# Kernel tuning notes

Hardware: AMD Instinct MI355X
Metric: run time of the kernel (lower is better)

The kernel has to match this reference:

```python
import jax, jax.numpy as jnp
import numpy as np

SCALES = (1, 2, 4)
KS = 5          # conv kernel size
POOL = 2        # maxpool kernel & stride


def coarse_grain(x, s):
    # non-overlapping mean pool along last axis
    B, C, L = x.shape
    Lc = L // s
    return x[:, :, : Lc * s].reshape(B, C, Lc, s).mean(axis=-1)


def conv1d(x, w, b):
    # x: [B, C_in, L], w: [C_out, C_in, K] (torch layout), VALID padding, stride 1
    y = jax.lax.conv_general_dilated(
        x, w, window_strides=(1,), padding='VALID',
        dimension_numbers=('NCH', 'OIH', 'NCH'))
    return y + b[None, :, None]


def maxpool1d(x, k):
    B, C, L = x.shape
    Lp = L // k
    return x[:, :, : Lp * k].reshape(B, C, Lp, k).max(axis=-1)


def conv_block(x, w1, b1, w2, b2):
    x = maxpool1d(jax.nn.relu(conv1d(x, w1, b1)), POOL)
    x = maxpool1d(jax.nn.relu(conv1d(x, w2, b2)), POOL)
    return x


def setup_inputs() -> dict:
    key = jax.random.key(0)
    ks = jax.random.split(key, 9)
    B, C, NWL = 2048, 4, 480
    C1, C2 = 16, 32
    # flatten size per model's own arithmetic: sum over scales of conv/pool output lens * C2
    F = (117 + 57 + 27) * C2  # 6432
    NOUT = 5
    sc = lambda fan_in: 1.0 / np.sqrt(fan_in)
    return {
        'x':  jax.random.normal(ks[0], (B, C, NWL), dtype=jnp.float32),
        'w1': jax.random.uniform(ks[1], (C1, C, KS), jnp.float32, -sc(C * KS), sc(C * KS)),
        'b1': jax.random.uniform(ks[2], (C1,), jnp.float32, -sc(C * KS), sc(C * KS)),
        'w2': jax.random.uniform(ks[3], (C2, C1, KS), jnp.float32, -sc(C1 * KS), sc(C1 * KS)),
        'b2': jax.random.uniform(ks[4], (C2,), jnp.float32, -sc(C1 * KS), sc(C1 * KS)),
        'wl': jax.random.uniform(ks[5], (F, F), jnp.float32, -sc(F), sc(F)),
        'bl': jax.random.uniform(ks[6], (F,), jnp.float32, -sc(F), sc(F)),
        'wo': jax.random.uniform(ks[7], (NOUT, F), jnp.float32, -sc(F), sc(F)),
        'bo': jax.random.uniform(ks[8], (NOUT,), jnp.float32, -sc(F), sc(F)),
    }


def reference(x, w1, b1, w2, b2, wl, bl, wo, bo):
    # multi-scale feature mapping: shared ConvBlock applied to each coarse-grained scale
    feats = [conv_block(coarse_grain(x, s), w1, b1, w2, b2) for s in SCALES]
    f = jnp.concatenate(feats, axis=-1)            # [B, 32, 201]
    f = f.reshape(f.shape[0], -1)                  # [B, 6432]
    # the SAME linear layer (shared weights) is applied 4 times in torch
    for _ in range(4):
        f = jax.nn.relu(f @ wl.T + bl)
    return f @ wo.T + bo                           # [B, 5]
```

## Files before the change

### kernel.cpp

```cpp
#include <hip/hip_runtime.h>

typedef _Float16 v8h __attribute__((ext_vector_type(8)));
typedef _Float16 v4h __attribute__((ext_vector_type(4)));
typedef float    v4f __attribute__((ext_vector_type(4)));

#define GK 6432
#define GN 6432
#define GM 2048
#define KP 6528

__global__ void convert_w(const float* __restrict__ wl, _Float16* __restrict__ Wh)
{
    const int row = blockIdx.y;
    const int col = (blockIdx.x * 256 + threadIdx.x) * 4;
    if (col >= KP) return;
    v4h h;
    if (col < GK) {
        const float4 f = *(const float4*)(wl + (long)row * GK + col);
        h[0] = (_Float16)f.x; h[1] = (_Float16)f.y;
        h[2] = (_Float16)f.z; h[3] = (_Float16)f.w;
    } else {
        h[0] = (_Float16)0.f; h[1] = (_Float16)0.f;
        h[2] = (_Float16)0.f; h[3] = (_Float16)0.f;
    }
    *(v4h*)(Wh + (long)row * KP + col) = h;
}

#define SX   0
#define SX2  2048
#define SX4  3136
#define SW1  3712
#define SB1  4032
#define SW2  4048
#define SB2  6608
#define SP1  6640
#define LDSZ 13808

__global__ __launch_bounds__(256) void conv_feat(
    const float* __restrict__ x,
    const float* __restrict__ w1, const float* __restrict__ b1,
    const float* __restrict__ w2, const float* __restrict__ b2,
    _Float16* __restrict__ F0)
{
    __shared__ float lds[LDSZ];
    const int tid = threadIdx.x;
    const long b  = blockIdx.x;

    for (int i = tid; i < 1920; i += 256) {
        int c = i / 480, t = i % 480;
        lds[SX + c * 512 + t] = x[(b * 4 + c) * 480 + t];
    }
    for (int i = tid; i < 320;  i += 256) lds[SW1 + i] = w1[i];
    for (int i = tid; i < 16;   i += 256) lds[SB1 + i] = b1[i];
    for (int i = tid; i < 2560; i += 256) lds[SW2 + i] = w2[i];
    for (int i = tid; i < 32;   i += 256) lds[SB2 + i] = b2[i];
    for (int i = tid; i < KP - GK; i += 256) F0[b * KP + GK + i] = (_Float16)0.f;
    __syncthreads();

    for (int i = tid; i < 960; i += 256) {
        int c = i / 240, t = i % 240;
        lds[SX2 + c * 272 + t] = 0.5f * (lds[SX + c * 512 + 2 * t] + lds[SX + c * 512 + 2 * t + 1]);
    }
    for (int i = tid; i < 480; i += 256) {
        int c = i / 120, t = i % 120;
        float s = lds[SX + c * 512 + 4 * t]     + lds[SX + c * 512 + 4 * t + 1]
                + lds[SX + c * 512 + 4 * t + 2] + lds[SX + c * 512 + 4 * t + 3];
        lds[SX4 + c * 144 + t] = 0.25f * s;
    }
    __syncthreads();

    for (int jid = tid; jid < 16 * 34; jid += 256) {
        const int c1 = jid / 34, rid = jid % 34;
        const int sidx = (rid < 19) ? 0 : (rid < 29 ? 1 : 2);
        const int r0   = (sidx == 0) ? rid : (sidx == 1 ? rid - 19 : rid - 29);
        const int u0   = r0 * 13;
        const int xbase  = (sidx == 0) ? SX  : (sidx == 1 ? SX2 : SX4);
        const int xpitch = (sidx == 0) ? 512 : (sidx == 1 ? 272 : 144);
        const int P      = (sidx == 0) ? 238 : (sidx == 1 ? 118 : 58);
        const int pofs   = (sidx == 0) ? 0   : (sidx == 1 ? 238 : 356);

        float acc[26];
        const float bias = lds[SB1 + c1];
        #pragma unroll
        for (int i = 0; i < 26; ++i) acc[i] = bias;

        #pragma unroll
        for (int ci = 0; ci < 4; ++ci) {
            float w[30];
            const float* xr = &lds[xbase + ci * xpitch + 2 * u0];
            #pragma unroll
            for (int q = 0; q < 15; ++q) {
                float2 t2 = *(const float2*)(xr + 2 * q);
                w[2 * q] = t2.x; w[2 * q + 1] = t2.y;
            }
            float wt[5];
            #pragma unroll
            for (int k = 0; k < 5; ++k) wt[k] = lds[SW1 + (c1 * 4 + ci) * 5 + k];
            #pragma unroll
            for (int i = 0; i < 26; ++i) {
                #pragma unroll
                for (int k = 0; k < 5; ++k) acc[i] += w[i + k] * wt[k];
            }
        }
        #pragma unroll
        for (int i = 0; i < 13; ++i) {
            int u = u0 + i;
            if (u < P)
                lds[SP1 + c1 * 448 + pofs + u] = fmaxf(fmaxf(acc[2 * i], acc[2 * i + 1]), 0.f);
        }
    }
    __syncthreads();

    for (int jid = tid; jid < 32 * 17; jid += 256) {
        const int c2 = jid / 17, rid = jid % 17;
        const int sidx = (rid < 9) ? 0 : (rid < 14 ? 1 : 2);
        const int r0   = (sidx == 0) ? rid : (sidx == 1 ? rid - 9 : rid - 14);
        const int v0   = r0 * 13;
        const int pbase = (sidx == 0) ? 0   : (sidx == 1 ? 238 : 356);
        const int Pv    = (sidx == 0) ? 117 : (sidx == 1 ? 57  : 27);
        const int vout  = (sidx == 0) ? 0   : (sidx == 1 ? 117 : 174);

        float acc[26];
        const float bias = lds[SB2 + c2];
        #pragma unroll
        for (int i = 0; i < 26; ++i) acc[i] = bias;

        for (int c1 = 0; c1 < 16; ++c1) {
            float w[30];
            const float* pr = &lds[SP1 + c1 * 448 + pbase + 2 * v0];
            #pragma unroll
            for (int q = 0; q < 15; ++q) {
                float2 t2 = *(const float2*)(pr + 2 * q);
                w[2 * q] = t2.x; w[2 * q + 1] = t2.y;
            }
            float wt[5];
            #pragma unroll
            for (int k = 0; k < 5; ++k) wt[k] = lds[SW2 + (c2 * 16 + c1) * 5 + k];
            #pragma unroll
            for (int i = 0; i < 26; ++i) {
                #pragma unroll
                for (int k = 0; k < 5; ++k) acc[i] += w[i + k] * wt[k];
            }
        }
        #pragma unroll
        for (int i = 0; i < 13; ++i) {
            int v = v0 + i;
            if (v < Pv) {
                float f = fmaxf(fmaxf(acc[2 * i], acc[2 * i + 1]), 0.f);
                F0[b * KP + c2 * 201 + vout + v] = (_Float16)f;
            }
        }
    }
}

__global__ __launch_bounds__(512, 2) void gemm8(
    const _Float16* __restrict__ A, const _Float16* __restrict__ Bw,
    const float* __restrict__ bias, _Float16* __restrict__ C)
{
    __shared__ _Float16 sA[2][256 * 64];
    __shared__ _Float16 sB[2][256 * 64];

    const int tid  = threadIdx.x;
    const int lane = tid & 63;
    const int wave = tid >> 6;
    const int wr   = wave >> 2;
    const int wc   = wave & 3;

    const int id  = blockIdx.x;
    const long tile_m = (long)(id & 7) << 8;
    const long tile_n = (long)(id >> 3) << 8;

    const int lrow = lane >> 3;
    const int lcol = ((lane & 7) ^ lrow) << 3;

    const int arow = wr * 128 + wc * 32;
    const int brow = wc * 64 + wr * 32;
    const _Float16* pA = A + (tile_m + arow + lrow) * (long)KP + lcol;
    long br0 = tile_n + brow + lrow;
    long br1 = br0 + 8, br2 = br0 + 16, br3 = br0 + 24;
    if (br0 > 6431) br0 = 6431;
    if (br1 > 6431) br1 = 6431;
    if (br2 > 6431) br2 = 6431;
    if (br3 > 6431) br3 = 6431;
    const _Float16* pB0 = Bw + br0 * (long)KP + lcol;
    const _Float16* pB1 = Bw + br1 * (long)KP + lcol;
    const _Float16* pB2 = Bw + br2 * (long)KP + lcol;
    const _Float16* pB3 = Bw + br3 * (long)KP + lcol;

    const int aDst = arow * 64;
    const int bDst = brow * 64;

#define GLD(p, d) __builtin_amdgcn_global_load_lds(                          \
        (const __attribute__((address_space(1))) void*)(p),                  \
        (__attribute__((address_space(3))) void*)(d), 16, 0, 0)

#define STAGE_A4(SBUF, KO) {                                                 \
    GLD(pA + (KO),            &sA[SBUF][aDst]);                              \
    GLD(pA + (KO) +  8L * KP, &sA[SBUF][aDst +  512]);                       \
    GLD(pA + (KO) + 16L * KP, &sA[SBUF][aDst + 1024]);                       \
    GLD(pA + (KO) + 24L * KP, &sA[SBUF][aDst + 1536]); }

#define STAGE_B4(SBUF, KO) {                                                 \
    GLD(pB0 + (KO), &sB[SBUF][bDst]);                                        \
    GLD(pB1 + (KO), &sB[SBUF][bDst +  512]);                                 \
    GLD(pB2 + (KO), &sB[SBUF][bDst + 1024]);                                 \
    GLD(pB3 + (KO), &sB[SBUF][bDst + 1536]); }

    const int fr = lane & 15;
    const int fp = lane >> 4;
    const int sw = fr & 7;
    const int slot0 = ((fp)     ^ sw) << 3;
    const int slot1 = ((fp + 4) ^ sw) << 3;
    const int abase = (wr * 128 + fr) * 64;
    const int boffS = (wc * 64 + fr) * 64 + wr * 2048;
    const int boffO = (wc * 64 + fr) * 64 + (1 - wr) * 2048;

    v8h af[4][2], bfO[2][2], bfs0[2][2], bfs1[2][2];
    v4f accS[8][2], accO[8][2];
    #pragma unroll
    for (int m = 0; m < 8; ++m) {
        #pragma unroll
        for (int ni = 0; ni < 2; ++ni) {
            v4f z = {0.f, 0.f, 0.f, 0.f};
            accS[m][ni] = z; accO[m][ni] = z;
        }
    }

#define LDA(CA, H) { _Pragma("unroll")                                       \
    for (int mi = 0; mi < 4; ++mi) {                                         \
        af[mi][0] = *(const v8h*)&(CA)[abase + (H) * 4096 + mi * 1024 + slot0]; \
        af[mi][1] = *(const v8h*)&(CA)[abase + (H) * 4096 + mi * 1024 + slot1]; \
    } }

#define LDBF(CB, BOFF, D) {                                                  \
    D[0][0] = *(const v8h*)&(CB)[(BOFF) + slot0];                            \
    D[0][1] = *(const v8h*)&(CB)[(BOFF) + slot1];                            \
    D[1][0] = *(const v8h*)&(CB)[(BOFF) + 1024 + slot0];                     \
    D[1][1] = *(const v8h*)&(CB)[(BOFF) + 1024 + slot1]; }

#define MMAQ(ACC, MH, BF) { _Pragma("unroll")                                \
    for (int mi = 0; mi < 4; ++mi) { _Pragma("unroll")                       \
        for (int ni = 0; ni < 2; ++ni) {                                     \
            ACC[(MH)*4+mi][ni] = __builtin_amdgcn_mfma_f32_16x16x32_f16(     \
                af[mi][0], BF[ni][0], ACC[(MH)*4+mi][ni], 0, 0, 0);          \
            ACC[(MH)*4+mi][ni] = __builtin_amdgcn_mfma_f32_16x16x32_f16(     \
                af[mi][1], BF[ni][1], ACC[(MH)*4+mi][ni], 0, 0, 0);          \
        } } }

#define ROUND(CA, CB, CBN, SBUF, KO, BFS, BFSN, S2, RA) {                    \
                                           \
    LDA(CA, 0);                                                              \
    __builtin_amdgcn_s_barrier();                                            \
    asm volatile("s_waitcnt lgkmcnt(0)" ::: "memory");                       \
    __builtin_amdgcn_s_setprio(1);                                           \
    MMAQ(accS, 0, BFS);                                                      \
    __builtin_amdgcn_s_setprio(0);                                           \
    __builtin_amdgcn_s_barrier();                                            \
                    \
    LDBF(CB, boffO, bfO);                                                    \
    if ((S2) && wc < 2) STAGE_A4(SBUF, KO);                                  \
    __builtin_amdgcn_s_barrier();                                            \
    asm volatile("s_waitcnt lgkmcnt(0)" ::: "memory");                       \
    __builtin_amdgcn_s_setprio(1);                                           \
    MMAQ(accO, 0, bfO);                                                      \
    __builtin_amdgcn_s_setprio(0);                                           \
    __builtin_amdgcn_s_barrier();                                            \
                            \
    LDA(CA, 1);                                                              \
    if (S2) STAGE_B4(SBUF, KO);                                              \
    __builtin_amdgcn_s_barrier();                                            \
    asm volatile("s_waitcnt lgkmcnt(0)" ::: "memory");                       \
    __builtin_amdgcn_s_setprio(1);                                           \
    MMAQ(accO, 1, bfO);                                                      \
    __builtin_amdgcn_s_setprio(0);                                           \
    __builtin_amdgcn_s_barrier();                                            \
    \
    if ((S2) && wc >= 2) STAGE_A4(SBUF, KO);                                 \
    __builtin_amdgcn_s_barrier();                                            \
    __builtin_amdgcn_s_setprio(1);                                           \
    MMAQ(accS, 1, BFS);                                                      \
    __builtin_amdgcn_s_setprio(0);                                           \
    if (S2) { asm volatile("s_waitcnt vmcnt(8)" ::: "memory"); }             \
    else    { asm volatile("s_waitcnt vmcnt(0)" ::: "memory"); }             \
    if (RA) LDBF(CBN, boffS, BFSN);                                          \
    __builtin_amdgcn_sched_barrier(0);                                       \
    __builtin_amdgcn_s_barrier(); }

    STAGE_A4(0, 0);  STAGE_B4(0, 0);
    STAGE_A4(1, 64); STAGE_B4(1, 64);
    pA += 128; pB0 += 128; pB1 += 128; pB2 += 128; pB3 += 128;
    asm volatile("s_waitcnt vmcnt(8)" ::: "memory");
    __builtin_amdgcn_s_barrier();
    LDBF(sB[0], boffS, bfs0);

    for (int kt = 0; kt < 102; kt += 2) {
        const bool s2a = kt < 100;
        const bool s2b = kt < 99;
        const bool raB = kt < 100;
        ROUND(sA[0], sB[0], sB[1], 0, 0,  bfs0, bfs1, s2a, true);
        ROUND(sA[1], sB[1], sB[0], 1, 64, bfs1, bfs0, s2b, raB);
        pA += 128; pB0 += 128; pB1 += 128; pB2 += 128; pB3 += 128;
    }

#define EPI(ACC, COL0) { _Pragma("unroll")                                   \
    for (int ni = 0; ni < 2; ++ni) {                                         \
        const long col = (COL0) + ni * 16;                                   \
        if (col < KP) {                                                      \
            const bool val = col < GN;                                       \
            const float bv = val ? bias[col] : 0.f;                          \
            _Pragma("unroll")                                                \
            for (int m = 0; m < 8; ++m) {                                    \
                const long row = tile_m + wr * 128 + m * 16 + fp * 4;        \
                _Pragma("unroll")                                            \
                for (int r = 0; r < 4; ++r) {                                \
                    float v = ACC[m][ni][r] + bv;                            \
                    v = v > 0.f ? v : 0.f;                                   \
                    C[(row + r) * (long)KP + col] = val ? (_Float16)v        \
                                                        : (_Float16)0.f;     \
                }                                                            \
            }                                                                \
        }                                                                    \
    } }

    const long colS0 = tile_n + wc * 64 + wr * 32 + fr;
    const long colO0 = tile_n + wc * 64 + (1 - wr) * 32 + fr;
    EPI(accS, colS0);
    EPI(accO, colO0);

#undef GLD
#undef STAGE_A4
#undef STAGE_B4
#undef LDA
#undef LDBF
#undef MMAQ
#undef ROUND
#undef EPI
}

__global__ __launch_bounds__(256) void final_out(
    const _Float16* __restrict__ F, const float* __restrict__ wo,
    const float* __restrict__ bo, float* __restrict__ out)
{
    __shared__ float red[4][8];
    const long b   = blockIdx.x;
    const int tid  = threadIdx.x;
    const int lane = tid & 63;
    const int wave = tid >> 6;
    float acc[5] = {0.f, 0.f, 0.f, 0.f, 0.f};
    const _Float16* f = F + b * KP;

    const int c1 = (wave + 1) * 402;
    for (int c = wave * 402 + lane; c < c1; c += 64) {
        const int k = c << 2;
        v4h f4 = *(const v4h*)(f + k);
        const float f0 = (float)f4[0], f1 = (float)f4[1];
        const float f2 = (float)f4[2], f3 = (float)f4[3];
        #pragma unroll
        for (int o = 0; o < 5; ++o) {
            const float4 w4 = *(const float4*)(wo + o * GK + k);
            acc[o] += f0 * w4.x + f1 * w4.y + f2 * w4.z + f3 * w4.w;
        }
    }
    #pragma unroll
    for (int o = 0; o < 5; ++o) {
        #pragma unroll
        for (int off = 32; off > 0; off >>= 1) acc[o] += __shfl_down(acc[o], off, 64);
    }
    if (lane == 0) {
        #pragma unroll
        for (int o = 0; o < 5; ++o) red[wave][o] = acc[o];
    }
    __syncthreads();
    if (tid < 5)
        out[b * 5 + tid] = red[0][tid] + red[1][tid] + red[2][tid] + red[3][tid] + bo[tid];
}

extern "C" void kernel_launch(void* const* d_in, const int* in_sizes, int n_in,
                              void* d_out, int out_size, void* d_ws, size_t ws_size,
                              hipStream_t stream)
{
    const float* x  = (const float*)d_in[0];
    const float* w1 = (const float*)d_in[1];
    const float* b1 = (const float*)d_in[2];
    const float* w2 = (const float*)d_in[3];
    const float* b2 = (const float*)d_in[4];
    const float* wl = (const float*)d_in[5];
    const float* bl = (const float*)d_in[6];
    const float* wo = (const float*)d_in[7];
    const float* bo = (const float*)d_in[8];
    float* out = (float*)d_out;

    char* ws = (char*)d_ws;
    _Float16* Wh = (_Float16*)ws;
    _Float16* F0 = (_Float16*)(ws + 83976192);
    _Float16* F1 = (_Float16*)(ws + 83976192 + 26738688);

    convert_w<<<dim3(7, GN), 256, 0, stream>>>(wl, Wh);
    conv_feat<<<GM, 256, 0, stream>>>(x, w1, b1, w2, b2, F0);
    gemm8<<<208, 512, 0, stream>>>(F0, Wh, bl, F1);
    gemm8<<<208, 512, 0, stream>>>(F1, Wh, bl, F0);
    gemm8<<<208, 512, 0, stream>>>(F0, Wh, bl, F1);
    gemm8<<<208, 512, 0, stream>>>(F1, Wh, bl, F0);
    final_out<<<GM, 256, 0, stream>>>(F0, wo, bo, out);
}
```

Measured before the change: 1.208 ms.

## Switch GEMM inner loop from 16x16x32 to 32x32x16 MFMA tiles

```diff
diff --git a/kernel.cpp b/kernel.cpp
--- a/kernel.cpp
+++ b/kernel.cpp
@@ -1,8 +1,8 @@
 #include <hip/hip_runtime.h>
 
-typedef _Float16 v8h __attribute__((ext_vector_type(8)));
-typedef _Float16 v4h __attribute__((ext_vector_type(4)));
-typedef float    v4f __attribute__((ext_vector_type(4)));
+typedef _Float16 v8h  __attribute__((ext_vector_type(8)));
+typedef _Float16 v4h  __attribute__((ext_vector_type(4)));
+typedef float    f32x16 __attribute__((ext_vector_type(16)));
 
 #define GK 6432
 #define GN 6432
@@ -206,84 +206,75 @@
     GLD(pB2 + (KO), &sB[SBUF][bDst + 1024]);                                 \
     GLD(pB3 + (KO), &sB[SBUF][bDst + 1536]); }
 
-    const int fr = lane & 15;
-    const int fp = lane >> 4;
-    const int sw = fr & 7;
-    const int slot0 = ((fp)     ^ sw) << 3;
-    const int slot1 = ((fp + 4) ^ sw) << 3;
-    const int abase = (wr * 128 + fr) * 64;
-    const int boffS = (wc * 64 + fr) * 64 + wr * 2048;
-    const int boffO = (wc * 64 + fr) * 64 + (1 - wr) * 2048;
-
-    v8h af[4][2], bfO[2][2], bfs0[2][2], bfs1[2][2];
-    v4f accS[8][2], accO[8][2];
+    const int fr32 = lane & 31;
+    const int g    = lane >> 5;
+    const int sw8  = lane & 7;
+    int q8[4];
     #pragma unroll
-    for (int m = 0; m < 8; ++m) {
-        #pragma unroll
-        for (int ni = 0; ni < 2; ++ni) {
-            v4f z = {0.f, 0.f, 0.f, 0.f};
-            accS[m][ni] = z; accO[m][ni] = z;
-        }
+    for (int s = 0; s < 4; ++s) q8[s] = (((2 * s + g) ^ sw8) << 3);
+
+    const int bS = wc * 64 + wr * 32;
+    const int bO = wc * 64 + (1 - wr) * 32;
+
+    v8h af[2][4], bfS[4], bfO[4];
+    f32x16 accS[4], accO[4];
+    #pragma unroll
+    for (int f = 0; f < 4; ++f) {
+        #pragma unroll
+        for (int r = 0; r < 16; ++r) { accS[f][r] = 0.f; accO[f][r] = 0.f; }
     }
 
 #define LDA(CA, H) { _Pragma("unroll")                                       \
-    for (int mi = 0; mi < 4; ++mi) {                                         \
-        af[mi][0] = *(const v8h*)&(CA)[abase + (H) * 4096 + mi * 1024 + slot0]; \
-        af[mi][1] = *(const v8h*)&(CA)[abase + (H) * 4096 + mi * 1024 + slot1]; \
+    for (int j = 0; j < 2; ++j) { _Pragma("unroll")                          \
+        for (int s = 0; s < 4; ++s)                                          \
+            af[j][s] = *(const v8h*)&(CA)[(wr * 128 + ((H) * 2 + j) * 32 + fr32) * 64 + q8[s]]; \
     } }
 
-#define LDBF(CB, BOFF, D) {                                                  \
-    D[0][0] = *(const v8h*)&(CB)[(BOFF) + slot0];                            \
-    D[0][1] = *(const v8h*)&(CB)[(BOFF) + slot1];                            \
-    D[1][0] = *(const v8h*)&(CB)[(BOFF) + 1024 + slot0];                     \
-    D[1][1] = *(const v8h*)&(CB)[(BOFF) + 1024 + slot1]; }
-
-#define MMAQ(ACC, MH, BF) { _Pragma("unroll")                                \
-    for (int mi = 0; mi < 4; ++mi) { _Pragma("unroll")                       \
-        for (int ni = 0; ni < 2; ++ni) {                                     \
-            ACC[(MH)*4+mi][ni] = __builtin_amdgcn_mfma_f32_16x16x32_f16(     \
-                af[mi][0], BF[ni][0], ACC[(MH)*4+mi][ni], 0, 0, 0);          \
-            ACC[(MH)*4+mi][ni] = __builtin_amdgcn_mfma_f32_16x16x32_f16(     \
-                af[mi][1], BF[ni][1], ACC[(MH)*4+mi][ni], 0, 0, 0);          \
-        } } }
-
-#define ROUND(CA, CB, CBN, SBUF, KO, BFS, BFSN, S2, RA) {                    \
-                                           \
-    LDA(CA, 0);                                                              \
+#define LDBF(CB, BROW, D) { _Pragma("unroll")                                \
+    for (int s = 0; s < 4; ++s)                                              \
+        D[s] = *(const v8h*)&(CB)[((BROW) + fr32) * 64 + q8[s]]; }
+
+#define MMAP(A0, A1, BF) { _Pragma("unroll")                                 \
+    for (int s = 0; s < 4; ++s) {                                            \
+        A0 = __builtin_amdgcn_mfma_f32_32x32x16_f16(af[0][s], BF[s], A0, 0, 0, 0); \
+        A1 = __builtin_amdgcn_mfma_f32_32x32x16_f16(af[1][s], BF[s], A1, 0, 0, 0); \
+    } }
+
+#define ROUND(CA, CB, SBUF, KO, S2) {                                        \
+                             \
+    LDBF(CB, bS, bfS); LDA(CA, 0);                                           \
     __builtin_amdgcn_s_barrier();                                            \
     asm volatile("s_waitcnt lgkmcnt(0)" ::: "memory");                       \
     __builtin_amdgcn_s_setprio(1);                                           \
-    MMAQ(accS, 0, BFS);                                                      \
+    MMAP(accS[0], accS[1], bfS);                                             \
     __builtin_amdgcn_s_setprio(0);                                           \
     __builtin_amdgcn_s_barrier();                                            \
-                    \
-    LDBF(CB, boffO, bfO);                                                    \
+                      \
+    LDBF(CB, bO, bfO);                                                       \
     if ((S2) && wc < 2) STAGE_A4(SBUF, KO);                                  \
     __builtin_amdgcn_s_barrier();                                            \
     asm volatile("s_waitcnt lgkmcnt(0)" ::: "memory");                       \
     __builtin_amdgcn_s_setprio(1);                                           \
-    MMAQ(accO, 0, bfO);                                                      \
+    MMAP(accO[0], accO[1], bfO);                                             \
     __builtin_amdgcn_s_setprio(0);                                           \
     __builtin_amdgcn_s_barrier();                                            \
-                            \
+                       \
     LDA(CA, 1);                                                              \
     if (S2) STAGE_B4(SBUF, KO);                                              \
     __builtin_amdgcn_s_barrier();                                            \
     asm volatile("s_waitcnt lgkmcnt(0)" ::: "memory");                       \
     __builtin_amdgcn_s_setprio(1);                                           \
-    MMAQ(accO, 1, bfO);                                                      \
+    MMAP(accO[2], accO[3], bfO);                                             \
     __builtin_amdgcn_s_setprio(0);                                           \
     __builtin_amdgcn_s_barrier();                                            \
-    \
+                \
     if ((S2) && wc >= 2) STAGE_A4(SBUF, KO);                                 \
     __builtin_amdgcn_s_barrier();                                            \
     __builtin_amdgcn_s_setprio(1);                                           \
-    MMAQ(accS, 1, BFS);                                                      \
+    MMAP(accS[2], accS[3], bfS);                                             \
     __builtin_amdgcn_s_setprio(0);                                           \
     if (S2) { asm volatile("s_waitcnt vmcnt(8)" ::: "memory"); }             \
     else    { asm volatile("s_waitcnt vmcnt(0)" ::: "memory"); }             \
-    if (RA) LDBF(CBN, boffS, BFSN);                                          \
-    __builtin_amdgcn_sched_barrier(0);                                       \
     __builtin_amdgcn_s_barrier(); }
 
     STAGE_A4(0, 0);  STAGE_B4(0, 0);
@@ -291,48 +282,38 @@
     pA += 128; pB0 += 128; pB1 += 128; pB2 += 128; pB3 += 128;
     asm volatile("s_waitcnt vmcnt(8)" ::: "memory");
     __builtin_amdgcn_s_barrier();
-    LDBF(sB[0], boffS, bfs0);
 
     for (int kt = 0; kt < 102; kt += 2) {
-        const bool s2a = kt < 100;
-        const bool s2b = kt < 99;
-        const bool raB = kt < 100;
-        ROUND(sA[0], sB[0], sB[1], 0, 0,  bfs0, bfs1, s2a, true);
-        ROUND(sA[1], sB[1], sB[0], 1, 64, bfs1, bfs0, s2b, raB);
+        ROUND(sA[0], sB[0], 0, 0,  kt < 100);
+        ROUND(sA[1], sB[1], 1, 64, kt < 99);
         pA += 128; pB0 += 128; pB1 += 128; pB2 += 128; pB3 += 128;
     }
 
-#define EPI(ACC, COL0) { _Pragma("unroll")                                   \
-    for (int ni = 0; ni < 2; ++ni) {                                         \
-        const long col = (COL0) + ni * 16;                                   \
-        if (col < KP) {                                                      \
-            const bool val = col < GN;                                       \
-            const float bv = val ? bias[col] : 0.f;                          \
-            _Pragma("unroll")                                                \
-            for (int m = 0; m < 8; ++m) {                                    \
-                const long row = tile_m + wr * 128 + m * 16 + fp * 4;        \
-                _Pragma("unroll")                                            \
-                for (int r = 0; r < 4; ++r) {                                \
-                    float v = ACC[m][ni][r] + bv;                            \
-                    v = v > 0.f ? v : 0.f;                                   \
-                    C[(row + r) * (long)KP + col] = val ? (_Float16)v        \
-                                                        : (_Float16)0.f;     \
-                }                                                            \
-            }                                                                \
-        }                                                                    \
-    } }
-
-    const long colS0 = tile_n + wc * 64 + wr * 32 + fr;
-    const long colO0 = tile_n + wc * 64 + (1 - wr) * 32 + fr;
-    EPI(accS, colS0);
-    EPI(accO, colO0);
+#define EPI(ACC, COL) {                                                      \
+    const bool val   = (COL) < GN;                                           \
+    const bool wr_ok = (COL) < KP;                                           \
+    const float bv = val ? bias[COL] : 0.f;                                  \
+    if (wr_ok) { _Pragma("unroll")                                           \
+        for (int f = 0; f < 4; ++f) { _Pragma("unroll")                      \
+            for (int r = 0; r < 16; ++r) {                                   \
+                const long row = tile_m + wr * 128 + f * 32                  \
+                               + (r & 3) + 8 * (r >> 2) + 4 * g;             \
+                float v = ACC[f][r] + bv;                                    \
+                v = v > 0.f ? v : 0.f;                                       \
+                C[row * (long)KP + (COL)] = val ? (_Float16)v : (_Float16)0.f; \
+            } } } }
+
+    const long colS = tile_n + bS + fr32;
+    const long colO = tile_n + bO + fr32;
+    EPI(accS, colS);
+    EPI(accO, colO);
 
 #undef GLD
 #undef STAGE_A4
 #undef STAGE_B4
 #undef LDA
 #undef LDBF
-#undef MMAQ
+#undef MMAP
 #undef ROUND
 #undef EPI
 }
```

Result: faster. 1.176 ms (-2.6%).

## Load GEMM B fragments directly from global into registers, skipping LDS staging

Applied to the files above, without the earlier changes.

```diff
diff --git a/kernel.cpp b/kernel.cpp
--- a/kernel.cpp
+++ b/kernel.cpp
@@ -153,12 +153,12 @@
     }
 }
 
-__global__ __launch_bounds__(512, 2) void gemm8(
+__global__ __launch_bounds__(512, 2) void gemm2p(
     const _Float16* __restrict__ A, const _Float16* __restrict__ Bw,
     const float* __restrict__ bias, _Float16* __restrict__ C)
 {
     __shared__ _Float16 sA[2][256 * 64];
-    __shared__ _Float16 sB[2][256 * 64];
+    __shared__ _Float16 ldspad[10240];
 
     const int tid  = threadIdx.x;
     const int lane = tid & 63;
@@ -166,56 +166,54 @@
     const int wr   = wave >> 2;
     const int wc   = wave & 3;
 
-    const int id  = blockIdx.x;
+    *(volatile _Float16*)&ldspad[tid] = (_Float16)0.f;
+
+    const int id = blockIdx.x;
     const long tile_m = (long)(id & 7) << 8;
     const long tile_n = (long)(id >> 3) << 8;
 
-    const int lrow = lane >> 3;
-    const int lcol = ((lane & 7) ^ lrow) << 3;
-
-    const int arow = wr * 128 + wc * 32;
-    const int brow = wc * 64 + wr * 32;
-    const _Float16* pA = A + (tile_m + arow + lrow) * (long)KP + lcol;
-    long br0 = tile_n + brow + lrow;
-    long br1 = br0 + 8, br2 = br0 + 16, br3 = br0 + 24;
-    if (br0 > 6431) br0 = 6431;
-    if (br1 > 6431) br1 = 6431;
-    if (br2 > 6431) br2 = 6431;
-    if (br3 > 6431) br3 = 6431;
-    const _Float16* pB0 = Bw + br0 * (long)KP + lcol;
-    const _Float16* pB1 = Bw + br1 * (long)KP + lcol;
-    const _Float16* pB2 = Bw + br2 * (long)KP + lcol;
-    const _Float16* pB3 = Bw + br3 * (long)KP + lcol;
-
-    const int aDst = arow * 64;
-    const int bDst = brow * 64;
+    const int lrow  = lane >> 3;
+    const int lcol  = ((lane & 7) ^ lrow) << 3;
+    const int base0 = wr * 128 + wc * 16;
+    const _Float16* pA0 = A + (tile_m + base0 + lrow) * (long)KP + lcol;
+    const _Float16* pA1 = pA0 + 64L * KP;
+    const int d00 = base0 * 64,        d01 = (base0 + 8) * 64;
+    const int d10 = (base0 + 64) * 64, d11 = (base0 + 72) * 64;
 
 #define GLD(p, d) __builtin_amdgcn_global_load_lds(                          \
         (const __attribute__((address_space(1))) void*)(p),                  \
         (__attribute__((address_space(3))) void*)(d), 16, 0, 0)
 
-#define STAGE_A4(SBUF, KO) {                                                 \
-    GLD(pA + (KO),            &sA[SBUF][aDst]);                              \
-    GLD(pA + (KO) +  8L * KP, &sA[SBUF][aDst +  512]);                       \
-    GLD(pA + (KO) + 16L * KP, &sA[SBUF][aDst + 1024]);                       \
-    GLD(pA + (KO) + 24L * KP, &sA[SBUF][aDst + 1536]); }
-
-#define STAGE_B4(SBUF, KO) {                                                 \
-    GLD(pB0 + (KO), &sB[SBUF][bDst]);                                        \
-    GLD(pB1 + (KO), &sB[SBUF][bDst +  512]);                                 \
-    GLD(pB2 + (KO), &sB[SBUF][bDst + 1024]);                                 \
-    GLD(pB3 + (KO), &sB[SBUF][bDst + 1536]); }
-
     const int fr = lane & 15;
     const int fp = lane >> 4;
-    const int sw = fr & 7;
+    long rS0 = tile_n + wc * 64 + wr * 32 + fr;
+    long rS1 = rS0 + 16;
+    long rO0 = tile_n + wc * 64 + (1 - wr) * 32 + fr;
+    long rO1 = rO0 + 16;
+    if (rS0 > 6431) rS0 = 6431;
+    if (rS1 > 6431) rS1 = 6431;
+    if (rO0 > 6431) rO0 = 6431;
+    if (rO1 > 6431) rO1 = 6431;
+    const _Float16* qS0 = Bw + rS0 * (long)KP + fp * 8;
+    const _Float16* qS1 = Bw + rS1 * (long)KP + fp * 8;
+    const _Float16* qO0 = Bw + rO0 * (long)KP + fp * 8;
+    const _Float16* qO1 = Bw + rO1 * (long)KP + fp * 8;
+
+    v8h bAS[2][2], bAO[2][2], bBS[2][2], bBO[2][2];
+
+#define LOADB(S, O) {                                                        \
+    S[0][0] = *(const v8h*)(qS0);      S[0][1] = *(const v8h*)(qS0 + 32);    \
+    S[1][0] = *(const v8h*)(qS1);      S[1][1] = *(const v8h*)(qS1 + 32);    \
+    O[0][0] = *(const v8h*)(qO0);      O[0][1] = *(const v8h*)(qO0 + 32);    \
+    O[1][0] = *(const v8h*)(qO1);      O[1][1] = *(const v8h*)(qO1 + 32);    \
+    qS0 += 64; qS1 += 64; qO0 += 64; qO1 += 64; }
+
+    const int sw    = fr & 7;
     const int slot0 = ((fp)     ^ sw) << 3;
     const int slot1 = ((fp + 4) ^ sw) << 3;
     const int abase = (wr * 128 + fr) * 64;
-    const int boffS = (wc * 64 + fr) * 64 + wr * 2048;
-    const int boffO = (wc * 64 + fr) * 64 + (1 - wr) * 2048;
-
-    v8h af[4][2], bfO[2][2], bfs0[2][2], bfs1[2][2];
+
+    v8h af[4][2];
     v4f accS[8][2], accO[8][2];
     #pragma unroll
     for (int m = 0; m < 8; ++m) {
@@ -231,12 +229,6 @@
         af[mi][0] = *(const v8h*)&(CA)[abase + (H) * 4096 + mi * 1024 + slot0]; \
         af[mi][1] = *(const v8h*)&(CA)[abase + (H) * 4096 + mi * 1024 + slot1]; \
     } }
-
-#define LDBF(CB, BOFF, D) {                                                  \
-    D[0][0] = *(const v8h*)&(CB)[(BOFF) + slot0];                            \
-    D[0][1] = *(const v8h*)&(CB)[(BOFF) + slot1];                            \
-    D[1][0] = *(const v8h*)&(CB)[(BOFF) + 1024 + slot0];                     \
-    D[1][1] = *(const v8h*)&(CB)[(BOFF) + 1024 + slot1]; }
 
 #define MMAQ(ACC, MH, BF) { _Pragma("unroll")                                \
     for (int mi = 0; mi < 4; ++mi) { _Pragma("unroll")                       \
@@ -247,60 +239,45 @@
                 af[mi][1], BF[ni][1], ACC[(MH)*4+mi][ni], 0, 0, 0);          \
         } } }
 
-#define ROUND(CA, CB, CBN, SBUF, KO, BFS, BFSN, S2, RA) {                    \
-                                           \
-    LDA(CA, 0);                                                              \
+    const _Float16* qA0 = pA0 + 128;
+    const _Float16* qA1 = pA1 + 64;
+
+#define ROUND(CB, BCS, BCO, BNS, BNO, S1, S0, VN) {                          \
+       \
+    LDA(sA[CB], 0);                                                          \
+    if (S1) { GLD(qA1, &sA[(CB)^1][d10]); GLD(qA1 + 8L*KP, &sA[(CB)^1][d11]); } \
+    if (S1) LOADB(BNS, BNO);                                                 \
     __builtin_amdgcn_s_barrier();                                            \
     asm volatile("s_waitcnt lgkmcnt(0)" ::: "memory");                       \
     __builtin_amdgcn_s_setprio(1);                                           \
-    MMAQ(accS, 0, BFS);                                                      \
+    MMAQ(accS, 0, BCS); MMAQ(accO, 0, BCO);                                  \
     __builtin_amdgcn_s_setprio(0);                                           \
     __builtin_amdgcn_s_barrier();                                            \
-                    \
-    LDBF(CB, boffO, bfO);                                                    \
-    if ((S2) && wc < 2) STAGE_A4(SBUF, KO);                                  \
+        \
+    if (S0) { GLD(qA0, &sA[CB][d00]); GLD(qA0 + 8L*KP, &sA[CB][d01]); }      \
+    LDA(sA[CB], 1);                                                          \
     __builtin_amdgcn_s_barrier();                                            \
     asm volatile("s_waitcnt lgkmcnt(0)" ::: "memory");                       \
     __builtin_amdgcn_s_setprio(1);                                           \
-    MMAQ(accO, 0, bfO);                                                      \
+    MMAQ(accS, 1, BCS); MMAQ(accO, 1, BCO);                                  \
     __builtin_amdgcn_s_setprio(0);                                           \
+    asm volatile("s_waitcnt vmcnt(" #VN ")" ::: "memory");                   \
     __builtin_amdgcn_s_barrier();                                            \
-                            \
-    LDA(CA, 1);                                                              \
-    if (S2) STAGE_B4(SBUF, KO);                                              \
-    __builtin_amdgcn_s_barrier();                                            \
-    asm volatile("s_waitcnt lgkmcnt(0)" ::: "memory");                       \
-    __builtin_amdgcn_s_setprio(1);                                           \
-    MMAQ(accO, 1, bfO);                                                      \
-    __builtin_amdgcn_s_setprio(0);                                           \
-    __builtin_amdgcn_s_barrier();                                            \
-    \
-    if ((S2) && wc >= 2) STAGE_A4(SBUF, KO);                                 \
-    __builtin_amdgcn_s_barrier();                                            \
-    __builtin_amdgcn_s_setprio(1);                                           \
-    MMAQ(accS, 1, BFS);                                                      \
-    __builtin_amdgcn_s_setprio(0);                                           \
-    if (S2) { asm volatile("s_waitcnt vmcnt(8)" ::: "memory"); }             \
-    else    { asm volatile("s_waitcnt vmcnt(0)" ::: "memory"); }             \
-    if (RA) LDBF(CBN, boffS, BFSN);                                          \
-    __builtin_amdgcn_sched_barrier(0);                                       \
-    __builtin_amdgcn_s_barrier(); }
-
-    STAGE_A4(0, 0);  STAGE_B4(0, 0);
-    STAGE_A4(1, 64); STAGE_B4(1, 64);
-    pA += 128; pB0 += 128; pB1 += 128; pB2 += 128; pB3 += 128;
-    asm volatile("s_waitcnt vmcnt(8)" ::: "memory");
+    qA0 += 64; qA1 += 64; }
+
+    GLD(pA0, &sA[0][d00]); GLD(pA0 + 8L * KP, &sA[0][d01]);
+    GLD(pA1, &sA[0][d10]); GLD(pA1 + 8L * KP, &sA[0][d11]);
+    LOADB(bAS, bAO);
+    GLD(pA0 + 64, &sA[1][d00]); GLD(pA0 + 64 + 8L * KP, &sA[1][d01]);
+    asm volatile("s_waitcnt vmcnt(0)" ::: "memory");
     __builtin_amdgcn_s_barrier();
-    LDBF(sB[0], boffS, bfs0);
-
-    for (int kt = 0; kt < 102; kt += 2) {
-        const bool s2a = kt < 100;
-        const bool s2b = kt < 99;
-        const bool raB = kt < 100;
-        ROUND(sA[0], sB[0], sB[1], 0, 0,  bfs0, bfs1, s2a, true);
-        ROUND(sA[1], sB[1], sB[0], 1, 64, bfs1, bfs0, s2b, raB);
-        pA += 128; pB0 += 128; pB1 += 128; pB2 += 128; pB3 += 128;
-    }
+
+    for (int kt = 0; kt < 100; kt += 2) {
+        ROUND(0, bAS, bAO, bBS, bBO, 1, 1, 2);
+        ROUND(1, bBS, bBO, bAS, bAO, 1, 1, 2);
+    }
+    ROUND(0, bAS, bAO, bBS, bBO, 1, 0, 0);
+    ROUND(1, bBS, bBO, bAS, bAO, 0, 0, 0);
 
 #define EPI(ACC, COL0) { _Pragma("unroll")                                   \
     for (int ni = 0; ni < 2; ++ni) {                                         \
@@ -328,10 +305,8 @@
     EPI(accO, colO0);
 
 #undef GLD
-#undef STAGE_A4
-#undef STAGE_B4
+#undef LOADB
 #undef LDA
-#undef LDBF
 #undef MMAQ
 #undef ROUND
 #undef EPI
@@ -397,9 +372,9 @@
 
     convert_w<<<dim3(7, GN), 256, 0, stream>>>(wl, Wh);
     conv_feat<<<GM, 256, 0, stream>>>(x, w1, b1, w2, b2, F0);
-    gemm8<<<208, 512, 0, stream>>>(F0, Wh, bl, F1);
-    gemm8<<<208, 512, 0, stream>>>(F1, Wh, bl, F0);
-    gemm8<<<208, 512, 0, stream>>>(F0, Wh, bl, F1);
-    gemm8<<<208, 512, 0, stream>>>(F1, Wh, bl, F0);
+    gemm2p<<<208, 512, 0, stream>>>(F0, Wh, bl, F1);
+    gemm2p<<<208, 512, 0, stream>>>(F1, Wh, bl, F0);
+    gemm2p<<<208, 512, 0, stream>>>(F0, Wh, bl, F1);
+    gemm2p<<<208, 512, 0, stream>>>(F1, Wh, bl, F0);
     final_out<<<GM, 256, 0, stream>>>(F0, wo, bo, out);
 }
```

New measurement: 1.617 ms. 33.9% more time.
